# Optimization experiments

Measured on AMD Instinct MI355X. Metric: run time of the kernel, lower is better.

Reference implementation:

```python
import jax, jax.numpy as jnp
import numpy as np
import math

NUM_HIDDEN = 512

def setup_inputs() -> dict:
    key = jax.random.key(0)
    k1, k2 = jax.random.split(key)
    a = jax.random.normal(k1, (8, 2048, NUM_HIDDEN), dtype=jnp.float32)
    b = jax.random.normal(k2, (8, 2048, NUM_HIDDEN), dtype=jnp.float32)
    return {"a": a, "b": b}

def reference(a, b):
    # simi_matrix: [B, La, Lb] = a @ b^T / sqrt(H)
    scale = 1.0 / math.sqrt(NUM_HIDDEN)
    simi = jnp.einsum('bld,bmd->blm', a, b) * scale
    norm_weight = jax.nn.softmax(simi, axis=2)
    # up_1: [B, La, H] = attn @ b + residual a
    up_1 = jnp.einsum('blm,bmd->bld', norm_weight, b) + a
    return up_1
```

## Files before the change

### kernel.cpp

```cpp
#include <hip/hip_runtime.h>
#include <hip/hip_bf16.h>

#define D 512
#define NSEQ 2048
#define NB 8
#define QBLK 64
#define KVBLK 64
#define NTHREADS 512
#define NT (NSEQ / KVBLK)
#define ROWE 2056
#define BUFE (16 * ROWE)
#define SROWP 68
#define PROWP 72

typedef __attribute__((ext_vector_type(8))) short bf16x8;
typedef __attribute__((ext_vector_type(4))) float f32x4;

static __device__ __forceinline__ unsigned short f2b(float f) {
  unsigned u = __builtin_bit_cast(unsigned, f);
  return (unsigned short)((u + 0x7FFFu + ((u >> 16) & 1u)) >> 16);
}

__global__ __launch_bounds__(256) void conv_b16(const float* __restrict__ in,
                                                unsigned short* __restrict__ out) {
  size_t i = ((size_t)blockIdx.x * 256 + threadIdx.x) * 8;
  float4 v0 = *reinterpret_cast<const float4*>(in + i);
  float4 v1 = *reinterpret_cast<const float4*>(in + i + 4);
  bf16x8 h;
  h[0] = (short)f2b(v0.x); h[1] = (short)f2b(v0.y);
  h[2] = (short)f2b(v0.z); h[3] = (short)f2b(v0.w);
  h[4] = (short)f2b(v1.x); h[5] = (short)f2b(v1.y);
  h[6] = (short)f2b(v1.z); h[7] = (short)f2b(v1.w);
  *reinterpret_cast<bf16x8*>(out + i) = h;
}

__global__ __launch_bounds__(NTHREADS, 1)
void attn_v10(const float* __restrict__ A, const unsigned short* __restrict__ B16,
              float* __restrict__ Out) {
  __shared__ __align__(16) unsigned short Bs[BUFE];
  __shared__ __align__(16) unsigned short Qs[BUFE];
  __shared__ __align__(16) float Ss[QBLK * SROWP];
  __shared__ __align__(16) unsigned short Ps[QBLK * PROWP];
  __shared__ float mS[QBLK];
  __shared__ float lS[QBLK];
  __shared__ float aS[QBLK];

  const int tid  = threadIdx.x;
  const int wid  = tid >> 6;
  const int lane = tid & 63;
  const int l16  = lane & 15;
  const int g4   = lane >> 4;

  const int batch = blockIdx.x & 7;
  const int qt    = blockIdx.x >> 3;
  const int qbase = qt * QBLK;

  const float*          Ab   = A   + (size_t)batch * NSEQ * D;
  const unsigned short* Bb16 = B16 + (size_t)batch * NSEQ * D;
  float*                Ob   = Out + (size_t)batch * NSEQ * D;

  const float scale = 0.04419417382415922f;

  const int ki = wid & 3;
  const int qp = wid >> 2;

  {
    const int q  = tid >> 3;
    const int dc = (tid & 7) * 64;
    const float* src = Ab + (size_t)(qbase + q) * D + dc;
    const int gbase = (q >> 2) * ROWE + (q & 3) * 16;
    #pragma unroll
    for (int j = 0; j < 8; ++j) {
      float4 v0 = *reinterpret_cast<const float4*>(src + j * 8);
      float4 v1 = *reinterpret_cast<const float4*>(src + j * 8 + 4);
      bf16x8 h;
      h[0] = (short)f2b(v0.x * scale); h[1] = (short)f2b(v0.y * scale);
      h[2] = (short)f2b(v0.z * scale); h[3] = (short)f2b(v0.w * scale);
      h[4] = (short)f2b(v1.x * scale); h[5] = (short)f2b(v1.y * scale);
      h[6] = (short)f2b(v1.z * scale); h[7] = (short)f2b(v1.w * scale);
      int d = dc + j * 8;
      *reinterpret_cast<bf16x8*>(&Qs[gbase + (d >> 4) * 64 + (d & 15)]) = h;
    }
  }
  if (tid < QBLK) { mS[tid] = -1e30f; lS[tid] = 0.f; }

  f32x4 acc[4][4];
  #pragma unroll
  for (int mi = 0; mi < 4; ++mi)
    #pragma unroll
    for (int ni = 0; ni < 4; ++ni)
      acc[mi][ni] = (f32x4){0.f, 0.f, 0.f, 0.f};

  #pragma unroll
  for (int c = 0; c < 8; ++c) {
    int id = wid * 8 + c;
    int g = id >> 2, q = id & 3;
    const unsigned short* src = Bb16
        + (size_t)(g * 4 + ((lane >> 1) & 3)) * D
        + q * 128 + (lane >> 3) * 16 + (lane & 1) * 8;
    unsigned short* dst = &Bs[g * ROWE + q * 512];
    __builtin_amdgcn_global_load_lds(
        (const __attribute__((address_space(1))) void*)src,
        (__attribute__((address_space(3))) void*)dst, 16, 0, 0);
  }
  asm volatile("s_waitcnt vmcnt(0)" ::: "memory");
  asm volatile("s_waitcnt lgkmcnt(0)" ::: "memory");
  __builtin_amdgcn_s_barrier();

  const int bbase = (ki * 4 + (l16 >> 2)) * ROWE + (l16 & 3) * 16 + (g4 & 1) * 8;
  const int qrb0  = ((qp * 2) * 4 + (l16 >> 2)) * ROWE + (l16 & 3) * 16 + (g4 & 1) * 8;
  const int qrb1  = qrb0 + 4 * ROWE;

  for (int kt = 0; kt < NT; ++kt) {
    {
      f32x4 s0 = {0.f, 0.f, 0.f, 0.f};
      f32x4 s1 = {0.f, 0.f, 0.f, 0.f};
      __builtin_amdgcn_s_setprio(1);
      #pragma unroll
      for (int ks = 0; ks < 16; ++ks) {
        const int ro = (ks * 2 + (g4 >> 1)) * 64;
        const bf16x8 bf = *reinterpret_cast<const bf16x8*>(&Bs[bbase + ro]);
        const bf16x8 q0 = *reinterpret_cast<const bf16x8*>(&Qs[qrb0 + ro]);
        const bf16x8 q1 = *reinterpret_cast<const bf16x8*>(&Qs[qrb1 + ro]);
        s0 = __builtin_amdgcn_mfma_f32_16x16x32_bf16(q0, bf, s0, 0, 0, 0);
        s1 = __builtin_amdgcn_mfma_f32_16x16x32_bf16(q1, bf, s1, 0, 0, 0);
      }
      __builtin_amdgcn_s_setprio(0);
      #pragma unroll
      for (int r = 0; r < 4; ++r) {
        Ss[(qp * 32 + g4 * 4 + r) * SROWP + ki * 16 + l16]      = s0[r];
        Ss[(qp * 32 + 16 + g4 * 4 + r) * SROWP + ki * 16 + l16] = s1[r];
      }
    }
    asm volatile("s_waitcnt lgkmcnt(0)" ::: "memory");
    __builtin_amdgcn_s_barrier();

    {
      int row = wid * 8 + (lane >> 3);
      int c8  = (lane & 7) * 8;
      float4 lo = *reinterpret_cast<const float4*>(&Ss[row * SROWP + c8]);
      float4 hi = *reinterpret_cast<const float4*>(&Ss[row * SROWP + c8 + 4]);
      float sv[8] = {lo.x, lo.y, lo.z, lo.w, hi.x, hi.y, hi.z, hi.w};
      float mloc = sv[0];
      #pragma unroll
      for (int j = 1; j < 8; ++j) mloc = fmaxf(mloc, sv[j]);
      #pragma unroll
      for (int off = 1; off < 8; off <<= 1)
        mloc = fmaxf(mloc, __shfl_xor(mloc, off));
      float mold = mS[row];
      float mnew = fmaxf(mold, mloc);
      float al = __expf(mold - mnew);
      float psum = 0.f;
      bf16x8 pw;
      #pragma unroll
      for (int j = 0; j < 8; ++j) {
        float p = __expf(sv[j] - mnew);
        psum += p;
        pw[j] = (short)f2b(p);
      }
      *reinterpret_cast<bf16x8*>(&Ps[row * PROWP + c8]) = pw;
      #pragma unroll
      for (int off = 1; off < 8; off <<= 1)
        psum += __shfl_xor(psum, off);
      if ((lane & 7) == 0) {
        mS[row] = mnew;
        lS[row] = lS[row] * al + psum;
        aS[row] = al;
      }
    }
    asm volatile("s_waitcnt lgkmcnt(0)" ::: "memory");
    __builtin_amdgcn_s_barrier();

    {
      #pragma unroll
      for (int mi = 0; mi < 4; ++mi)
        #pragma unroll
        for (int r = 0; r < 4; ++r) {
          float a = aS[mi * 16 + g4 * 4 + r];
          #pragma unroll
          for (int ni = 0; ni < 4; ++ni)
            acc[mi][ni][r] *= a;
        }

      const unsigned short* Bc = &Bs[0];
      __builtin_amdgcn_s_setprio(1);
      #pragma unroll
      for (int ks = 0; ks < 2; ++ks) {
        bf16x8 pf[4];
        #pragma unroll
        for (int mi = 0; mi < 4; ++mi)
          pf[mi] = *reinterpret_cast<const bf16x8*>(
              &Ps[(mi * 16 + l16) * PROWP + ks * 32 + g4 * 8]);
        #pragma unroll
        for (int ni = 0; ni < 4; ++ni) {
          bf16x8 vv;
          #pragma unroll
          for (int j = 0; j < 8; ++j)
            vv[j] = (short)Bc[(ks * 8 + g4 * 2 + (j >> 2)) * ROWE
                              + (wid * 4 + ni) * 64 + (j & 3) * 16 + l16];
          #pragma unroll
          for (int mi = 0; mi < 4; ++mi)
            acc[mi][ni] = __builtin_amdgcn_mfma_f32_16x16x32_bf16(pf[mi], vv, acc[mi][ni], 0, 0, 0);
        }
      }
      __builtin_amdgcn_s_setprio(0);
    }

    __builtin_amdgcn_s_barrier();
    if (kt + 1 < NT) {
      const unsigned short* Bt = Bb16 + (size_t)(kt + 1) * KVBLK * D;
      #pragma unroll
      for (int c = 0; c < 8; ++c) {
        int id = wid * 8 + c;
        int g = id >> 2, q = id & 3;
        const unsigned short* src = Bt
            + (size_t)(g * 4 + ((lane >> 1) & 3)) * D
            + q * 128 + (lane >> 3) * 16 + (lane & 1) * 8;
        unsigned short* dst = &Bs[g * ROWE + q * 512];
        __builtin_amdgcn_global_load_lds(
            (const __attribute__((address_space(1))) void*)src,
            (__attribute__((address_space(3))) void*)dst, 16, 0, 0);
      }
      asm volatile("s_waitcnt vmcnt(0)" ::: "memory");
    }
    __builtin_amdgcn_s_barrier();
  }

  #pragma unroll
  for (int mi = 0; mi < 4; ++mi)
    #pragma unroll
    for (int r = 0; r < 4; ++r) {
      float rl = 1.0f / lS[mi * 16 + g4 * 4 + r];
      #pragma unroll
      for (int ni = 0; ni < 4; ++ni) {
        int q = qbase + mi * 16 + g4 * 4 + r;
        int d = wid * 64 + ni * 16 + l16;
        size_t off = (size_t)q * D + d;
        Ob[off] = acc[mi][ni][r] * rl + Ab[off];
      }
    }
}

#define FQBLK 32
#define FSROWP (64 + 4)
#define FPROWP (64 + 8)
__global__ __launch_bounds__(NTHREADS, 2)
void attn_fb(const float* __restrict__ A, const float* __restrict__ B32,
             float* __restrict__ Out) {
  __shared__ __align__(16) unsigned short Bs[BUFE];
  __shared__ float Ss[FQBLK * FSROWP];
  __shared__ unsigned short Ps[FQBLK * FPROWP];
  __shared__ float mS[FQBLK];
  __shared__ float lS[FQBLK];
  __shared__ float aS[FQBLK];

  const int tid  = threadIdx.x;
  const int wid  = tid >> 6;
  const int lane = tid & 63;
  const int l16  = lane & 15;
  const int g4   = lane >> 4;

  const int batch = blockIdx.x & 7;
  const int qt    = blockIdx.x >> 3;
  const int qbase = qt * FQBLK;

  const float* Ab   = A   + (size_t)batch * NSEQ * D;
  const float* Bb32 = B32 + (size_t)batch * NSEQ * D;
  float*       Ob   = Out + (size_t)batch * NSEQ * D;

  const float scale = 0.04419417382415922f;

  const int qi = wid >> 2;
  const int ki = wid & 3;

  const float* Arow = Ab + (size_t)(qbase + qi * 16 + l16) * D;
  bf16x8 qf[16];
  #pragma unroll
  for (int ks = 0; ks < 16; ++ks) {
    int d0 = ks * 32 + g4 * 8;
    float4 v0 = *reinterpret_cast<const float4*>(Arow + d0);
    float4 v1 = *reinterpret_cast<const float4*>(Arow + d0 + 4);
    bf16x8 f;
    f[0] = (short)f2b(v0.x * scale); f[1] = (short)f2b(v0.y * scale);
    f[2] = (short)f2b(v0.z * scale); f[3] = (short)f2b(v0.w * scale);
    f[4] = (short)f2b(v1.x * scale); f[5] = (short)f2b(v1.y * scale);
    f[6] = (short)f2b(v1.z * scale); f[7] = (short)f2b(v1.w * scale);
    qf[ks] = f;
  }
  if (tid < FQBLK) { mS[tid] = -1e30f; lS[tid] = 0.f; }

  f32x4 acc[2][4];
  #pragma unroll
  for (int mi = 0; mi < 2; ++mi)
    #pragma unroll
    for (int ni = 0; ni < 4; ++ni)
      acc[mi][ni] = (f32x4){0.f, 0.f, 0.f, 0.f};

  for (int kt = 0; kt < NT; ++kt) {
    __builtin_amdgcn_s_barrier();
    const float* Bt = Bb32 + (size_t)kt * KVBLK * D;
    #pragma unroll
    for (int c = 0; c < 8; ++c) {
      int id = wid * 8 + c;
      int g = id >> 2, q = id & 3;
      int kv = g * 4 + ((lane >> 1) & 3);
      int d  = q * 128 + (lane >> 3) * 16 + (lane & 1) * 8;
      const float* s = Bt + (size_t)kv * D + d;
      float4 v0 = *reinterpret_cast<const float4*>(s);
      float4 v1 = *reinterpret_cast<const float4*>(s + 4);
      bf16x8 h;
      h[0] = (short)f2b(v0.x); h[1] = (short)f2b(v0.y);
      h[2] = (short)f2b(v0.z); h[3] = (short)f2b(v0.w);
      h[4] = (short)f2b(v1.x); h[5] = (short)f2b(v1.y);
      h[6] = (short)f2b(v1.z); h[7] = (short)f2b(v1.w);
      *reinterpret_cast<bf16x8*>(&Bs[g * ROWE + q * 512 + lane * 8]) = h;
    }
    asm volatile("s_waitcnt lgkmcnt(0)" ::: "memory");
    __builtin_amdgcn_s_barrier();

    {
      f32x4 s = {0.f, 0.f, 0.f, 0.f};
      const int bbase = (ki * 4 + (l16 >> 2)) * ROWE + (l16 & 3) * 16 + (g4 & 1) * 8;
      #pragma unroll
      for (int ks = 0; ks < 16; ++ks) {
        const bf16x8 bf = *reinterpret_cast<const bf16x8*>(
            &Bs[bbase + (ks * 2 + (g4 >> 1)) * 64]);
        s = __builtin_amdgcn_mfma_f32_16x16x32_bf16(qf[ks], bf, s, 0, 0, 0);
      }
      #pragma unroll
      for (int r = 0; r < 4; ++r)
        Ss[(qi * 16 + g4 * 4 + r) * FSROWP + ki * 16 + l16] = s[r];
    }
    asm volatile("s_waitcnt lgkmcnt(0)" ::: "memory");
    __builtin_amdgcn_s_barrier();

    {
      int row = wid * 4 + g4;
      float sv[4];
      float mloc = -1e30f;
      #pragma unroll
      for (int j = 0; j < 4; ++j) {
        sv[j] = Ss[row * FSROWP + l16 + 16 * j];
        mloc = fmaxf(mloc, sv[j]);
      }
      #pragma unroll
      for (int off = 1; off < 16; off <<= 1)
        mloc = fmaxf(mloc, __shfl_xor(mloc, off));
      float mold = mS[row];
      float mnew = fmaxf(mold, mloc);
      float al = __expf(mold - mnew);
      float psum = 0.f;
      #pragma unroll
      for (int j = 0; j < 4; ++j) {
        float p = __expf(sv[j] - mnew);
        psum += p;
        Ps[row * FPROWP + l16 + 16 * j] = f2b(p);
      }
      #pragma unroll
      for (int off = 1; off < 16; off <<= 1)
        psum += __shfl_xor(psum, off);
      if (l16 == 0) {
        mS[row] = mnew;
        lS[row] = lS[row] * al + psum;
        aS[row] = al;
      }
    }
    asm volatile("s_waitcnt lgkmcnt(0)" ::: "memory");
    __builtin_amdgcn_s_barrier();

    {
      #pragma unroll
      for (int mi = 0; mi < 2; ++mi)
        #pragma unroll
        for (int r = 0; r < 4; ++r) {
          float a = aS[mi * 16 + g4 * 4 + r];
          #pragma unroll
          for (int ni = 0; ni < 4; ++ni)
            acc[mi][ni][r] *= a;
        }

      #pragma unroll
      for (int ks = 0; ks < 2; ++ks) {
        bf16x8 pf[2];
        #pragma unroll
        for (int mi = 0; mi < 2; ++mi)
          pf[mi] = *reinterpret_cast<const bf16x8*>(
              &Ps[(mi * 16 + l16) * FPROWP + ks * 32 + g4 * 8]);
        #pragma unroll
        for (int ni = 0; ni < 4; ++ni) {
          bf16x8 vv;
          #pragma unroll
          for (int j = 0; j < 8; ++j)
            vv[j] = (short)Bs[(ks * 8 + g4 * 2 + (j >> 2)) * ROWE
                              + (wid * 4 + ni) * 64 + (j & 3) * 16 + l16];
          #pragma unroll
          for (int mi = 0; mi < 2; ++mi)
            acc[mi][ni] = __builtin_amdgcn_mfma_f32_16x16x32_bf16(pf[mi], vv, acc[mi][ni], 0, 0, 0);
        }
      }
    }
  }

  #pragma unroll
  for (int mi = 0; mi < 2; ++mi)
    #pragma unroll
    for (int r = 0; r < 4; ++r) {
      float rl = 1.0f / lS[mi * 16 + g4 * 4 + r];
      #pragma unroll
      for (int ni = 0; ni < 4; ++ni) {
        int q = qbase + mi * 16 + g4 * 4 + r;
        int d = wid * 64 + ni * 16 + l16;
        size_t off = (size_t)q * D + d;
        Ob[off] = acc[mi][ni][r] * rl + Ab[off];
      }
    }
}

extern "C" void kernel_launch(void* const* d_in, const int* in_sizes, int n_in,
                              void* d_out, int out_size, void* d_ws, size_t ws_size,
                              hipStream_t stream) {
  const float* a = (const float*)d_in[0];
  const float* b = (const float*)d_in[1];
  float* out = (float*)d_out;
  const size_t need = (size_t)NB * NSEQ * D * sizeof(unsigned short);
  dim3 block(NTHREADS);
  if (ws_size >= need) {
    unsigned short* b16 = (unsigned short*)d_ws;
    conv_b16<<<4096, 256, 0, stream>>>(b, b16);
    dim3 grid(NB * (NSEQ / QBLK));
    attn_v10<<<grid, block, 0, stream>>>(a, b16, out);
  } else {
    dim3 grid(NB * (NSEQ / FQBLK));
    attn_fb<<<grid, block, 0, stream>>>(a, b, out);
  }
}
```

Measured before the change: 163.9 us.

## Pretranspose B to bf16, register-stream K and vectorize swizzled V loads

The conversion kernel now emits both a row-major bf16 copy of B and a transposed bf16 copy via an LDS tile transpose. The attention kernel streams K fragments straight from global memory into registers, prefetching the next tile, instead of staging them in LDS. It stages V from the transposed copy with an XOR swizzle so the P·V operand is one 16-byte LDS read rather than eight scalar gathers. The MFMA operand order is swapped so results land transposed, which enables float4 epilogue loads and stores. The cost is a doubled workspace requirement, extra transpose traffic and higher register pressure from holding K fragments.

```diff
diff --git a/kernel.cpp b/kernel.cpp
--- a/kernel.cpp
+++ b/kernel.cpp
@@ -12,33 +12,79 @@
 #define BUFE (16 * ROWE)
 #define SROWP 68
 #define PROWP 72
+#define CROWP 68
 
 typedef __attribute__((ext_vector_type(8))) short bf16x8;
 typedef __attribute__((ext_vector_type(4))) float f32x4;
+typedef __attribute__((ext_vector_type(4))) unsigned short u16x4;
 
 static __device__ __forceinline__ unsigned short f2b(float f) {
   unsigned u = __builtin_bit_cast(unsigned, f);
   return (unsigned short)((u + 0x7FFFu + ((u >> 16) & 1u)) >> 16);
 }
 
-__global__ __launch_bounds__(256) void conv_b16(const float* __restrict__ in,
-                                                unsigned short* __restrict__ out) {
-  size_t i = ((size_t)blockIdx.x * 256 + threadIdx.x) * 8;
-  float4 v0 = *reinterpret_cast<const float4*>(in + i);
-  float4 v1 = *reinterpret_cast<const float4*>(in + i + 4);
-  bf16x8 h;
-  h[0] = (short)f2b(v0.x); h[1] = (short)f2b(v0.y);
-  h[2] = (short)f2b(v0.z); h[3] = (short)f2b(v0.w);
-  h[4] = (short)f2b(v1.x); h[5] = (short)f2b(v1.y);
-  h[6] = (short)f2b(v1.z); h[7] = (short)f2b(v1.w);
-  *reinterpret_cast<bf16x8*>(out + i) = h;
+__global__ __launch_bounds__(256) void conv_dual(const float* __restrict__ in,
+                                                 unsigned short* __restrict__ b16,
+                                                 unsigned short* __restrict__ bT) {
+  __shared__ unsigned short tile[64 * CROWP];
+  const int bid = blockIdx.x;
+  const int batch = bid >> 8;
+  const int rem = bid & 255;
+  const int kvt = rem >> 3;
+  const int dt  = rem & 7;
+  const int t = threadIdx.x;
+  const int r = t >> 2;
+  const int c = (t & 3) * 16;
+
+  const float* src = in + ((size_t)batch * NSEQ + kvt * 64 + r) * D + dt * 64 + c;
+  unsigned short* o16 = b16 + ((size_t)batch * NSEQ + kvt * 64 + r) * D + dt * 64 + c;
+
+  float4 v0 = *reinterpret_cast<const float4*>(src);
+  float4 v1 = *reinterpret_cast<const float4*>(src + 4);
+  float4 v2 = *reinterpret_cast<const float4*>(src + 8);
+  float4 v3 = *reinterpret_cast<const float4*>(src + 12);
+  bf16x8 h0, h1;
+  h0[0] = (short)f2b(v0.x); h0[1] = (short)f2b(v0.y);
+  h0[2] = (short)f2b(v0.z); h0[3] = (short)f2b(v0.w);
+  h0[4] = (short)f2b(v1.x); h0[5] = (short)f2b(v1.y);
+  h0[6] = (short)f2b(v1.z); h0[7] = (short)f2b(v1.w);
+  h1[0] = (short)f2b(v2.x); h1[1] = (short)f2b(v2.y);
+  h1[2] = (short)f2b(v2.z); h1[3] = (short)f2b(v2.w);
+  h1[4] = (short)f2b(v3.x); h1[5] = (short)f2b(v3.y);
+  h1[6] = (short)f2b(v3.z); h1[7] = (short)f2b(v3.w);
+  *reinterpret_cast<bf16x8*>(o16)     = h0;
+  *reinterpret_cast<bf16x8*>(o16 + 8) = h1;
+  #pragma unroll
+  for (int i = 0; i < 4; ++i) {
+    u16x4 w;
+    w[0] = (unsigned short)((i < 2 ? h0 : h1)[(i & 1) * 4 + 0]);
+    w[1] = (unsigned short)((i < 2 ? h0 : h1)[(i & 1) * 4 + 1]);
+    w[2] = (unsigned short)((i < 2 ? h0 : h1)[(i & 1) * 4 + 2]);
+    w[3] = (unsigned short)((i < 2 ? h0 : h1)[(i & 1) * 4 + 3]);
+    *reinterpret_cast<u16x4*>(&tile[r * CROWP + c + i * 4]) = w;
+  }
+  __syncthreads();
+
+  const int w  = t >> 6;
+  const int dr = t & 63;
+  unsigned short* oT = bT + (size_t)batch * D * NSEQ
+                          + (size_t)(dt * 64 + dr) * NSEQ + kvt * 64 + w * 16;
+  unsigned short g[16];
+  #pragma unroll
+  for (int i = 0; i < 16; ++i)
+    g[i] = tile[(w * 16 + i) * CROWP + dr];
+  bf16x8 p0, p1;
+  #pragma unroll
+  for (int i = 0; i < 8; ++i) { p0[i] = (short)g[i]; p1[i] = (short)g[8 + i]; }
+  *reinterpret_cast<bf16x8*>(oT)     = p0;
+  *reinterpret_cast<bf16x8*>(oT + 8) = p1;
 }
 
 __global__ __launch_bounds__(NTHREADS, 1)
-void attn_v10(const float* __restrict__ A, const unsigned short* __restrict__ B16,
-              float* __restrict__ Out) {
-  __shared__ __align__(16) unsigned short Bs[BUFE];
+void attn_v11(const float* __restrict__ A, const unsigned short* __restrict__ K16,
+              const unsigned short* __restrict__ T16, float* __restrict__ Out) {
   __shared__ __align__(16) unsigned short Qs[BUFE];
+  __shared__ __align__(16) unsigned short Bt[D * KVBLK];
   __shared__ __align__(16) float Ss[QBLK * SROWP];
   __shared__ __align__(16) unsigned short Ps[QBLK * PROWP];
   __shared__ float mS[QBLK];
@@ -55,9 +101,10 @@
   const int qt    = blockIdx.x >> 3;
   const int qbase = qt * QBLK;
 
-  const float*          Ab   = A   + (size_t)batch * NSEQ * D;
-  const unsigned short* Bb16 = B16 + (size_t)batch * NSEQ * D;
-  float*                Ob   = Out + (size_t)batch * NSEQ * D;
+  const float*          Ab = A   + (size_t)batch * NSEQ * D;
+  const unsigned short* Kb = K16 + (size_t)batch * NSEQ * D;
+  const unsigned short* Tb = T16 + (size_t)batch * D * NSEQ;
+  float*                Ob = Out + (size_t)batch * NSEQ * D;
 
   const float scale = 0.04419417382415922f;
 
@@ -84,6 +131,12 @@
   }
   if (tid < QBLK) { mS[tid] = -1e30f; lS[tid] = 0.f; }
 
+  const unsigned short* kptr = Kb + (size_t)(ki * 16 + l16) * D + g4 * 8;
+  bf16x8 kf[16];
+  #pragma unroll
+  for (int ks = 0; ks < 16; ++ks)
+    kf[ks] = *reinterpret_cast<const bf16x8*>(kptr + ks * 32);
+
   f32x4 acc[4][4];
   #pragma unroll
   for (int mi = 0; mi < 4; ++mi)
@@ -93,12 +146,10 @@
 
   #pragma unroll
   for (int c = 0; c < 8; ++c) {
-    int id = wid * 8 + c;
-    int g = id >> 2, q = id & 3;
-    const unsigned short* src = Bb16
-        + (size_t)(g * 4 + ((lane >> 1) & 3)) * D
-        + q * 128 + (lane >> 3) * 16 + (lane & 1) * 8;
-    unsigned short* dst = &Bs[g * ROWE + q * 512];
+    int drow = wid * 64 + c * 8 + (lane >> 3);
+    int chunk = (lane & 7) ^ ((lane >> 3) & 7);
+    const unsigned short* src = Tb + (size_t)drow * NSEQ + chunk * 8;
+    unsigned short* dst = (unsigned short*)&Bt[(wid * 64 + c * 8) * KVBLK];
     __builtin_amdgcn_global_load_lds(
         (const __attribute__((address_space(1))) void*)src,
         (__attribute__((address_space(3))) void*)dst, 16, 0, 0);
@@ -107,9 +158,8 @@
   asm volatile("s_waitcnt lgkmcnt(0)" ::: "memory");
   __builtin_amdgcn_s_barrier();
 
-  const int bbase = (ki * 4 + (l16 >> 2)) * ROWE + (l16 & 3) * 16 + (g4 & 1) * 8;
-  const int qrb0  = ((qp * 2) * 4 + (l16 >> 2)) * ROWE + (l16 & 3) * 16 + (g4 & 1) * 8;
-  const int qrb1  = qrb0 + 4 * ROWE;
+  const int qrb0 = ((qp * 2) * 4 + (l16 >> 2)) * ROWE + (l16 & 3) * 16 + (g4 & 1) * 8;
+  const int qrb1 = qrb0 + 4 * ROWE;
 
   for (int kt = 0; kt < NT; ++kt) {
     {
@@ -119,11 +169,10 @@
       #pragma unroll
       for (int ks = 0; ks < 16; ++ks) {
         const int ro = (ks * 2 + (g4 >> 1)) * 64;
-        const bf16x8 bf = *reinterpret_cast<const bf16x8*>(&Bs[bbase + ro]);
         const bf16x8 q0 = *reinterpret_cast<const bf16x8*>(&Qs[qrb0 + ro]);
         const bf16x8 q1 = *reinterpret_cast<const bf16x8*>(&Qs[qrb1 + ro]);
-        s0 = __builtin_amdgcn_mfma_f32_16x16x32_bf16(q0, bf, s0, 0, 0, 0);
-        s1 = __builtin_amdgcn_mfma_f32_16x16x32_bf16(q1, bf, s1, 0, 0, 0);
+        s0 = __builtin_amdgcn_mfma_f32_16x16x32_bf16(q0, kf[ks], s0, 0, 0, 0);
+        s1 = __builtin_amdgcn_mfma_f32_16x16x32_bf16(q1, kf[ks], s1, 0, 0, 0);
       }
       __builtin_amdgcn_s_setprio(0);
       #pragma unroll
@@ -134,6 +183,13 @@
     }
     asm volatile("s_waitcnt lgkmcnt(0)" ::: "memory");
     __builtin_amdgcn_s_barrier();
+
+    if (kt + 1 < NT) {
+      kptr += (size_t)KVBLK * D;
+      #pragma unroll
+      for (int ks = 0; ks < 16; ++ks)
+        kf[ks] = *reinterpret_cast<const bf16x8*>(kptr + ks * 32);
+    }
 
     {
       int row = wid * 8 + (lane >> 3);
@@ -173,16 +229,16 @@
 
     {
       #pragma unroll
-      for (int mi = 0; mi < 4; ++mi)
-        #pragma unroll
-        for (int r = 0; r < 4; ++r) {
-          float a = aS[mi * 16 + g4 * 4 + r];
+      for (int mi = 0; mi < 4; ++mi) {
+        float a = aS[mi * 16 + l16];
+        #pragma unroll
+        for (int ni = 0; ni < 4; ++ni)
           #pragma unroll
-          for (int ni = 0; ni < 4; ++ni)
+          for (int r = 0; r < 4; ++r)
             acc[mi][ni][r] *= a;
-        }
-
-      const unsigned short* Bc = &Bs[0];
+      }
+
+      const char* Bc = (const char*)&Bt[0];
       __builtin_amdgcn_s_setprio(1);
       #pragma unroll
       for (int ks = 0; ks < 2; ++ks) {
@@ -193,30 +249,26 @@
               &Ps[(mi * 16 + l16) * PROWP + ks * 32 + g4 * 8]);
         #pragma unroll
         for (int ni = 0; ni < 4; ++ni) {
-          bf16x8 vv;
-          #pragma unroll
-          for (int j = 0; j < 8; ++j)
-            vv[j] = (short)Bc[(ks * 8 + g4 * 2 + (j >> 2)) * ROWE
-                              + (wid * 4 + ni) * 64 + (j & 3) * 16 + l16];
+          int row = wid * 64 + ni * 16 + l16;
+          int swz = (ks * 4 + g4) ^ (l16 & 7);
+          const bf16x8 vf = *reinterpret_cast<const bf16x8*>(Bc + row * 128 + swz * 16);
           #pragma unroll
           for (int mi = 0; mi < 4; ++mi)
-            acc[mi][ni] = __builtin_amdgcn_mfma_f32_16x16x32_bf16(pf[mi], vv, acc[mi][ni], 0, 0, 0);
+            acc[mi][ni] = __builtin_amdgcn_mfma_f32_16x16x32_bf16(vf, pf[mi], acc[mi][ni], 0, 0, 0);
         }
       }
       __builtin_amdgcn_s_setprio(0);
     }
 
+    asm volatile("s_waitcnt lgkmcnt(0)" ::: "memory");
     __builtin_amdgcn_s_barrier();
     if (kt + 1 < NT) {
-      const unsigned short* Bt = Bb16 + (size_t)(kt + 1) * KVBLK * D;
       #pragma unroll
       for (int c = 0; c < 8; ++c) {
-        int id = wid * 8 + c;
-        int g = id >> 2, q = id & 3;
-        const unsigned short* src = Bt
-            + (size_t)(g * 4 + ((lane >> 1) & 3)) * D
-            + q * 128 + (lane >> 3) * 16 + (lane & 1) * 8;
-        unsigned short* dst = &Bs[g * ROWE + q * 512];
+        int drow = wid * 64 + c * 8 + (lane >> 3);
+        int chunk = (lane & 7) ^ ((lane >> 3) & 7);
+        const unsigned short* src = Tb + (size_t)drow * NSEQ + (kt + 1) * KVBLK + chunk * 8;
+        unsigned short* dst = (unsigned short*)&Bt[(wid * 64 + c * 8) * KVBLK];
         __builtin_amdgcn_global_load_lds(
             (const __attribute__((address_space(1))) void*)src,
             (__attribute__((address_space(3))) void*)dst, 16, 0, 0);
@@ -227,18 +279,21 @@
   }
 
   #pragma unroll
-  for (int mi = 0; mi < 4; ++mi)
-    #pragma unroll
-    for (int r = 0; r < 4; ++r) {
-      float rl = 1.0f / lS[mi * 16 + g4 * 4 + r];
-      #pragma unroll
-      for (int ni = 0; ni < 4; ++ni) {
-        int q = qbase + mi * 16 + g4 * 4 + r;
-        int d = wid * 64 + ni * 16 + l16;
-        size_t off = (size_t)q * D + d;
-        Ob[off] = acc[mi][ni][r] * rl + Ab[off];
-      }
-    }
+  for (int mi = 0; mi < 4; ++mi) {
+    float rl = 1.0f / lS[mi * 16 + l16];
+    int q = qbase + mi * 16 + l16;
+    #pragma unroll
+    for (int ni = 0; ni < 4; ++ni) {
+      int d = wid * 64 + ni * 16 + g4 * 4;
+      const float4 av = *reinterpret_cast<const float4*>(Ab + (size_t)q * D + d);
+      float4 o;
+      o.x = acc[mi][ni][0] * rl + av.x;
+      o.y = acc[mi][ni][1] * rl + av.y;
+      o.z = acc[mi][ni][2] * rl + av.z;
+      o.w = acc[mi][ni][3] * rl + av.w;
+      *reinterpret_cast<float4*>(Ob + (size_t)q * D + d) = o;
+    }
+  }
 }
 
 #define FQBLK 32
@@ -298,14 +353,14 @@
 
   for (int kt = 0; kt < NT; ++kt) {
     __builtin_amdgcn_s_barrier();
-    const float* Bt = Bb32 + (size_t)kt * KVBLK * D;
+    const float* Bt2 = Bb32 + (size_t)kt * KVBLK * D;
     #pragma unroll
     for (int c = 0; c < 8; ++c) {
       int id = wid * 8 + c;
       int g = id >> 2, q = id & 3;
       int kv = g * 4 + ((lane >> 1) & 3);
       int d  = q * 128 + (lane >> 3) * 16 + (lane & 1) * 8;
-      const float* s = Bt + (size_t)kv * D + d;
+      const float* s = Bt2 + (size_t)kv * D + d;
       float4 v0 = *reinterpret_cast<const float4*>(s);
       float4 v1 = *reinterpret_cast<const float4*>(s + 4);
       bf16x8 h;
@@ -422,13 +477,14 @@
   const float* a = (const float*)d_in[0];
   const float* b = (const float*)d_in[1];
   float* out = (float*)d_out;
-  const size_t need = (size_t)NB * NSEQ * D * sizeof(unsigned short);
+  const size_t one = (size_t)NB * NSEQ * D * sizeof(unsigned short);
   dim3 block(NTHREADS);
-  if (ws_size >= need) {
+  if (ws_size >= 2 * one) {
     unsigned short* b16 = (unsigned short*)d_ws;
-    conv_b16<<<4096, 256, 0, stream>>>(b, b16);
+    unsigned short* bT  = b16 + (size_t)NB * NSEQ * D;
+    conv_dual<<<NB * 256, 256, 0, stream>>>(b, b16, bT);
     dim3 grid(NB * (NSEQ / QBLK));
-    attn_v10<<<grid, block, 0, stream>>>(a, b16, out);
+    attn_v11<<<grid, block, 0, stream>>>(a, b16, bT, out);
   } else {
     dim3 grid(NB * (NSEQ / FQBLK));
     attn_fb<<<grid, block, 0, stream>>>(a, b, out);
```

New measurement: 212.2 us. 29.5% more time.

## Load QK^T B-operand fragments directly from global into registers with prefetch

Applied to the files above, without the earlier changes.

The S=QK^T stage now reads its B operand (bf16 keys) straight from global memory into a 16-entry register array per wave, instead of from the shared-memory B tile. The next tile's fragments are prefetched right after the score barrier, so the load overlaps the softmax and PV stages. The softmax pass also changes its Ss/Ps access from contiguous 8-wide vectors to strided scalar accesses, likely to reduce LDS bank conflicts. This raises VGPR pressure by 64 registers and issues narrow, uncoalesced global loads that hit L2 repeatedly.

```diff
diff --git a/kernel.cpp b/kernel.cpp
--- a/kernel.cpp
+++ b/kernel.cpp
@@ -35,7 +35,7 @@
 }
 
 __global__ __launch_bounds__(NTHREADS, 1)
-void attn_v10(const float* __restrict__ A, const unsigned short* __restrict__ B16,
+void attn_v12(const float* __restrict__ A, const unsigned short* __restrict__ B16,
               float* __restrict__ Out) {
   __shared__ __align__(16) unsigned short Bs[BUFE];
   __shared__ __align__(16) unsigned short Qs[BUFE];
@@ -84,6 +84,12 @@
   }
   if (tid < QBLK) { mS[tid] = -1e30f; lS[tid] = 0.f; }
 
+  const unsigned short* kptr = Bb16 + (size_t)(ki * 16 + l16) * D + g4 * 8;
+  bf16x8 kf[16];
+  #pragma unroll
+  for (int ks = 0; ks < 16; ++ks)
+    kf[ks] = *reinterpret_cast<const bf16x8*>(kptr + ks * 32);
+
   f32x4 acc[4][4];
   #pragma unroll
   for (int mi = 0; mi < 4; ++mi)
@@ -107,9 +113,8 @@
   asm volatile("s_waitcnt lgkmcnt(0)" ::: "memory");
   __builtin_amdgcn_s_barrier();
 
-  const int bbase = (ki * 4 + (l16 >> 2)) * ROWE + (l16 & 3) * 16 + (g4 & 1) * 8;
-  const int qrb0  = ((qp * 2) * 4 + (l16 >> 2)) * ROWE + (l16 & 3) * 16 + (g4 & 1) * 8;
-  const int qrb1  = qrb0 + 4 * ROWE;
+  const int qrb0 = ((qp * 2) * 4 + (l16 >> 2)) * ROWE + (l16 & 3) * 16 + (g4 & 1) * 8;
+  const int qrb1 = qrb0 + 4 * ROWE;
 
   for (int kt = 0; kt < NT; ++kt) {
     {
@@ -119,11 +124,10 @@
       #pragma unroll
       for (int ks = 0; ks < 16; ++ks) {
         const int ro = (ks * 2 + (g4 >> 1)) * 64;
-        const bf16x8 bf = *reinterpret_cast<const bf16x8*>(&Bs[bbase + ro]);
         const bf16x8 q0 = *reinterpret_cast<const bf16x8*>(&Qs[qrb0 + ro]);
         const bf16x8 q1 = *reinterpret_cast<const bf16x8*>(&Qs[qrb1 + ro]);
-        s0 = __builtin_amdgcn_mfma_f32_16x16x32_bf16(q0, bf, s0, 0, 0, 0);
-        s1 = __builtin_amdgcn_mfma_f32_16x16x32_bf16(q1, bf, s1, 0, 0, 0);
+        s0 = __builtin_amdgcn_mfma_f32_16x16x32_bf16(q0, kf[ks], s0, 0, 0, 0);
+        s1 = __builtin_amdgcn_mfma_f32_16x16x32_bf16(q1, kf[ks], s1, 0, 0, 0);
       }
       __builtin_amdgcn_s_setprio(0);
       #pragma unroll
@@ -135,15 +139,23 @@
     asm volatile("s_waitcnt lgkmcnt(0)" ::: "memory");
     __builtin_amdgcn_s_barrier();
 
+    if (kt + 1 < NT) {
+      kptr += (size_t)KVBLK * D;
+      #pragma unroll
+      for (int ks = 0; ks < 16; ++ks)
+        kf[ks] = *reinterpret_cast<const bf16x8*>(kptr + ks * 32);
+    }
+
     {
       int row = wid * 8 + (lane >> 3);
-      int c8  = (lane & 7) * 8;
-      float4 lo = *reinterpret_cast<const float4*>(&Ss[row * SROWP + c8]);
-      float4 hi = *reinterpret_cast<const float4*>(&Ss[row * SROWP + c8 + 4]);
-      float sv[8] = {lo.x, lo.y, lo.z, lo.w, hi.x, hi.y, hi.z, hi.w};
-      float mloc = sv[0];
-      #pragma unroll
-      for (int j = 1; j < 8; ++j) mloc = fmaxf(mloc, sv[j]);
+      int c   = lane & 7;
+      float sv[8];
+      float mloc = -1e30f;
+      #pragma unroll
+      for (int j = 0; j < 8; ++j) {
+        sv[j] = Ss[row * SROWP + c + 8 * j];
+        mloc = fmaxf(mloc, sv[j]);
+      }
       #pragma unroll
       for (int off = 1; off < 8; off <<= 1)
         mloc = fmaxf(mloc, __shfl_xor(mloc, off));
@@ -151,18 +163,16 @@
       float mnew = fmaxf(mold, mloc);
       float al = __expf(mold - mnew);
       float psum = 0.f;
-      bf16x8 pw;
       #pragma unroll
       for (int j = 0; j < 8; ++j) {
         float p = __expf(sv[j] - mnew);
         psum += p;
-        pw[j] = (short)f2b(p);
-      }
-      *reinterpret_cast<bf16x8*>(&Ps[row * PROWP + c8]) = pw;
+        Ps[row * PROWP + c + 8 * j] = f2b(p);
+      }
       #pragma unroll
       for (int off = 1; off < 8; off <<= 1)
         psum += __shfl_xor(psum, off);
-      if ((lane & 7) == 0) {
+      if (c == 0) {
         mS[row] = mnew;
         lS[row] = lS[row] * al + psum;
         aS[row] = al;
@@ -298,14 +308,14 @@
 
   for (int kt = 0; kt < NT; ++kt) {
     __builtin_amdgcn_s_barrier();
-    const float* Bt = Bb32 + (size_t)kt * KVBLK * D;
+    const float* Bt2 = Bb32 + (size_t)kt * KVBLK * D;
     #pragma unroll
     for (int c = 0; c < 8; ++c) {
       int id = wid * 8 + c;
       int g = id >> 2, q = id & 3;
       int kv = g * 4 + ((lane >> 1) & 3);
       int d  = q * 128 + (lane >> 3) * 16 + (lane & 1) * 8;
-      const float* s = Bt + (size_t)kv * D + d;
+      const float* s = Bt2 + (size_t)kv * D + d;
       float4 v0 = *reinterpret_cast<const float4*>(s);
       float4 v1 = *reinterpret_cast<const float4*>(s + 4);
       bf16x8 h;
@@ -428,7 +438,7 @@
     unsigned short* b16 = (unsigned short*)d_ws;
     conv_b16<<<4096, 256, 0, stream>>>(b, b16);
     dim3 grid(NB * (NSEQ / QBLK));
-    attn_v10<<<grid, block, 0, stream>>>(a, b16, out);
+    attn_v12<<<grid, block, 0, stream>>>(a, b16, out);
   } else {
     dim3 grid(NB * (NSEQ / FQBLK));
     attn_fb<<<grid, block, 0, stream>>>(a, b, out);
```

Result: slower. 223.9 us (+36.6%).
